# Optimization experiments

Hardware: AMD Instinct MI355X
Metric: run time of the kernel (lower is better)

The kernel has to match this reference:

```python
import jax, jax.numpy as jnp
import numpy as np

NUM_USR = 8192
H = 256  # NUM_SOURCE == H (feature dim of y_a); NUM_TARGET = 256


def setup_inputs() -> dict:
    key = jax.random.key(0)
    k1, k2, k3, k4 = jax.random.split(key, 4)
    return {
        "y_a": jax.random.normal(k1, (NUM_USR, H), dtype=jnp.float32),
        "y_b": jax.random.normal(k2, (NUM_USR, H), dtype=jnp.float32),
        "W": jax.random.normal(k3, (H, H), dtype=jnp.float32) * (1.0 / np.sqrt(H)),
        "b": jax.random.normal(k4, (H,), dtype=jnp.float32) * 0.01,
    }


def reference(y_a, y_b, W, b):
    # Linear: proj[j] = W @ y_b[j] + b   (torch nn.Linear convention)
    proj = jnp.einsum("jt,st->js", y_b, W) + b          # [num_usr, H]
    # torch loop computes score[i, j] = y_a[i] . proj[j], replicated H times
    # then averaged: out[i, k] = (1/H) * sum_j sigmoid(score[i, j])
    scores = jnp.einsum("ih,jh->ij", y_a, proj)          # [num_usr, num_usr]
    s = jnp.sum(jax.nn.sigmoid(scores), axis=1) / y_a.shape[1]  # [num_usr]
    return jnp.broadcast_to(s[:, None], y_a.shape)       # [num_usr, H]
```

## Files before the change

### kernel.cpp

```cpp
#include <hip/hip_runtime.h>

#define NUSR 8192
#define HDIM 256

typedef __attribute__((ext_vector_type(8))) __bf16 bf16x8;
typedef __attribute__((ext_vector_type(4))) float f32x4;

union frag_u { bf16x8 v; unsigned short u[8]; unsigned int d[4]; };

__device__ __forceinline__ unsigned int f2bf(float f) {
  unsigned u = __builtin_bit_cast(unsigned, f);
  u += 0x7FFFu + ((u >> 16) & 1u);
  return u >> 16;
}
__device__ __forceinline__ unsigned int f2bf2(float lo, float hi) {
  return f2bf(lo) | (f2bf(hi) << 16);
}
__device__ __forceinline__ float sigmoidf_fast(float x) {
  float e = __builtin_amdgcn_exp2f(x * -1.44269504088896340736f);
  return __builtin_amdgcn_rcpf(1.0f + e);
}


__global__ __launch_bounds__(256) void k1_fused(
    const float* __restrict__ ya, const float* __restrict__ yb,
    const float* __restrict__ W, const float* __restrict__ bvec,
    unsigned short* __restrict__ yabf, unsigned short* __restrict__ PX,
    float* __restrict__ svec, unsigned int* __restrict__ done)
{
  const int b   = blockIdx.x;
  const int tid = threadIdx.x;

  if (b < 128) {
    const int lane = tid & 63;
    const int w    = tid >> 6;
    const int q    = lane >> 4;
    const int i    = lane & 15;

    frag_u B[4][8];
#pragma unroll
    for (int g = 0; g < 4; ++g) {
      const float* ybrow = yb + (size_t)(b * 64 + g * 16 + i) * HDIM;
#pragma unroll
      for (int kb = 0; kb < 8; ++kb) {
        float4 v0 = *(const float4*)&ybrow[kb * 32 + q * 8];
        float4 v1 = *(const float4*)&ybrow[kb * 32 + q * 8 + 4];
        B[g][kb].d[0] = f2bf2(v0.x, v0.y); B[g][kb].d[1] = f2bf2(v0.z, v0.w);
        B[g][kb].d[2] = f2bf2(v1.x, v1.y); B[g][kb].d[3] = f2bf2(v1.z, v1.w);
      }
    }

#pragma unroll
    for (int t = 0; t < 4; ++t) {
      const int st = w * 4 + t;
      f32x4 acc[4] = {{0.f,0.f,0.f,0.f},{0.f,0.f,0.f,0.f},
                      {0.f,0.f,0.f,0.f},{0.f,0.f,0.f,0.f}};
#pragma unroll
      for (int kb = 0; kb < 8; ++kb) {
        const float* wr = W + (size_t)(st * 16 + i) * HDIM + kb * 32 + q * 8;
        float4 w0 = *(const float4*)wr;
        float4 w1 = *(const float4*)(wr + 4);
        frag_u Af;
        Af.d[0] = f2bf2(w0.x, w0.y); Af.d[1] = f2bf2(w0.z, w0.w);
        Af.d[2] = f2bf2(w1.x, w1.y); Af.d[3] = f2bf2(w1.z, w1.w);
#pragma unroll
        for (int g = 0; g < 4; ++g)
          acc[g] = __builtin_amdgcn_mfma_f32_16x16x32_bf16(Af.v, B[g][kb].v, acc[g], 0, 0, 0);
      }
      float4 bias = *(const float4*)&bvec[st * 16 + q * 4];
#pragma unroll
      for (int g = 0; g < 4; ++g) {
        const int jg = b * 4 + g;
        unsigned v0 = f2bf2(acc[g][0] + bias.x, acc[g][1] + bias.y);
        unsigned v1 = f2bf2(acc[g][2] + bias.z, acc[g][3] + bias.w);
        size_t off = (size_t)jg * 4096 + (size_t)(st >> 1) * 512
                   + (size_t)(((st & 1) << 1) | (q >> 1)) * 128 + i * 8 + ((q & 1) * 4);
        *(uint2*)(PX + off) = make_uint2(v0, v1);
      }
    }
  } else {
    const int id = (b - 128) * 256 + tid;
    const float4* src = (const float4*)ya;
    uint4* dst = (uint4*)yabf;
#pragma unroll
    for (int u = 0; u < 3; ++u) {
      int d = id + u * 98304;
      if (d < 262144) {
        float4 a = src[d * 2];
        float4 c = src[d * 2 + 1];
        uint4 o = { f2bf2(a.x, a.y), f2bf2(a.z, a.w),
                    f2bf2(c.x, c.y), f2bf2(c.z, c.w) };
        dst[d] = o;
      }
    }
    if (b == 511) {
      float4 z = {0.f, 0.f, 0.f, 0.f};
      float4* sv = (float4*)svec;
#pragma unroll
      for (int u = 0; u < 8; ++u) sv[u * 256 + tid] = z;
      if (tid < 32) done[tid] = 0u;
    }
  }
}

__global__ __launch_bounds__(256, 2) void k2_score(
    const unsigned short* __restrict__ yabf, const unsigned short* __restrict__ PX,
    float* __restrict__ svec, unsigned int* __restrict__ done,
    float* __restrict__ out, const int fuse_tail)
{
  __shared__ __align__(16) unsigned short bs[2][8192];
  __shared__ unsigned int lastv;
  const int tid  = threadIdx.x;
  const int lane = tid & 63;
  const int w    = tid >> 6;
  const int quad = lane >> 4;
  const int l15  = lane & 15;
  const int rbase = blockIdx.x * 256 + w * 64;
  const int cg16  = blockIdx.y * 32;

  frag_u A[4][8];
#pragma unroll
  for (int g = 0; g < 4; ++g) {
    const unsigned short* src = yabf + (size_t)(rbase + g * 16 + l15) * HDIM;
#pragma unroll
    for (int kb = 0; kb < 8; ++kb)
      A[g][kb].v = *(const bf16x8*)&src[kb * 32 + quad * 8];
  }

  const unsigned short* psrc = PX + (size_t)cg16 * 4096;

  float rs[4][4] = {{0.f,0.f,0.f,0.f},{0.f,0.f,0.f,0.f},
                    {0.f,0.f,0.f,0.f},{0.f,0.f,0.f,0.f}};

#pragma unroll
  for (int p = 0; p < 4; ++p) {
    int c = p * 256 + tid;
    __builtin_amdgcn_global_load_lds(
        (const __attribute__((address_space(1))) unsigned int*)(const void*)(psrc + c * 8),
        (__attribute__((address_space(3))) unsigned int*)(void*)(&bs[0][0] + c * 8),
        16, 0, 0);
  }
  __syncthreads();

  for (int t = 0; t < 16; ++t) {
    if (t < 15) {
      const unsigned short* src = psrc + (size_t)(t + 1) * 8192;
      unsigned short* dst = &bs[(t + 1) & 1][0];
#pragma unroll
      for (int p = 0; p < 4; ++p) {
        int c = p * 256 + tid;
        __builtin_amdgcn_global_load_lds(
            (const __attribute__((address_space(1))) unsigned int*)(const void*)(src + c * 8),
            (__attribute__((address_space(3))) unsigned int*)(void*)(dst + c * 8),
            16, 0, 0);
      }
    }
    const unsigned short* buf = &bs[t & 1][0];
#pragma unroll
    for (int tt = 0; tt < 2; ++tt) {
      f32x4 acc[4] = {{0.f,0.f,0.f,0.f},{0.f,0.f,0.f,0.f},
                      {0.f,0.f,0.f,0.f},{0.f,0.f,0.f,0.f}};
#pragma unroll
      for (int kb = 0; kb < 8; ++kb) {
        bf16x8 bfrag = *(const bf16x8*)&buf[(tt * 512 + kb * 64 + lane) * 8];
#pragma unroll
        for (int g = 0; g < 4; ++g)
          acc[g] = __builtin_amdgcn_mfma_f32_16x16x32_bf16(A[g][kb].v, bfrag, acc[g], 0, 0, 0);
      }
#pragma unroll
      for (int g = 0; g < 4; ++g)
#pragma unroll
        for (int r = 0; r < 4; ++r)
          rs[g][r] += sigmoidf_fast(acc[g][r]);
    }
    __syncthreads();
  }

#pragma unroll
  for (int off = 1; off < 16; off <<= 1)
#pragma unroll
    for (int g = 0; g < 4; ++g)
#pragma unroll
      for (int r = 0; r < 4; ++r)
        rs[g][r] += __shfl_xor(rs[g][r], off, 64);

  if (l15 == 0) {
#pragma unroll
    for (int g = 0; g < 4; ++g)
#pragma unroll
      for (int r = 0; r < 4; ++r)
        atomicAdd(&svec[rbase + g * 16 + quad * 4 + r], rs[g][r]);
  }

  if (!fuse_tail) return;

  __syncthreads();
  if (tid == 0)
    lastv = __hip_atomic_fetch_add(&done[blockIdx.x], 1u,
                                   __ATOMIC_ACQ_REL, __HIP_MEMORY_SCOPE_AGENT);
  __syncthreads();
  if (lastv == 15u) {
    const int rb = blockIdx.x * 256;
    const float inv = 1.0f / 256.0f;
#pragma unroll 4
    for (int u = 0; u < 64; ++u) {
      int row = u * 4 + w;
      float s = __hip_atomic_load(&svec[rb + row],
                                  __ATOMIC_RELAXED, __HIP_MEMORY_SCOPE_AGENT);
      float v = s * inv;
      float4 o = {v, v, v, v};
      ((float4*)out)[(size_t)(rb + row) * 64 + lane] = o;
    }
  }
}

__global__ __launch_bounds__(256) void k3_bcast(
    const float* __restrict__ svec, float* __restrict__ out)
{
  int idx = blockIdx.x * 256 + threadIdx.x;
  int row = idx >> 6;
  float v = svec[row] * (1.0f / 256.0f);
  float4 o = {v, v, v, v};
  ((float4*)out)[idx] = o;
}

extern "C" void kernel_launch(void* const* d_in, const int* in_sizes, int n_in,
                              void* d_out, int out_size, void* d_ws, size_t ws_size,
                              hipStream_t stream) {
  (void)in_sizes; (void)n_in; (void)out_size;
  const float* ya = (const float*)d_in[0];
  const float* yb = (const float*)d_in[1];
  const float* W  = (const float*)d_in[2];
  const float* bv = (const float*)d_in[3];
  float* out = (float*)d_out;

  char* ws = (char*)d_ws;
  unsigned short *PX, *yabf;
  float* svec;
  unsigned int* done;
  int fuse;
  const size_t need = (8ull << 20) + (64ull << 10);
  if (ws_size >= need) {
    PX   = (unsigned short*)ws;
    yabf = (unsigned short*)(ws + (4 << 20));
    svec = (float*)(ws + (8 << 20));
    done = (unsigned int*)(ws + (8 << 20) + (32 << 10));
    fuse = 1;
  } else {
    PX   = (unsigned short*)d_out;
    yabf = (unsigned short*)((char*)d_out + (4 << 20));
    svec = (float*)ws;
    done = (unsigned int*)(ws + (32 << 10));
    fuse = 0;
  }

  k1_fused<<<512, 256, 0, stream>>>(ya, yb, W, bv, yabf, PX, svec, done);
  k2_score<<<dim3(32, 16), 256, 0, stream>>>(yabf, PX, svec, done, out, fuse);
  if (!fuse) k3_bcast<<<2048, 256, 0, stream>>>(svec, out);
}
```

Baseline: 138.7 us.

## Load score-kernel B fragments directly to registers, remap blocks per XCD, drop fused tail

```diff
diff --git a/kernel.cpp b/kernel.cpp
--- a/kernel.cpp
+++ b/kernel.cpp
@@ -26,21 +26,21 @@
     const float* __restrict__ ya, const float* __restrict__ yb,
     const float* __restrict__ W, const float* __restrict__ bvec,
     unsigned short* __restrict__ yabf, unsigned short* __restrict__ PX,
-    float* __restrict__ svec, unsigned int* __restrict__ done)
+    float* __restrict__ svec)
 {
   const int b   = blockIdx.x;
   const int tid = threadIdx.x;
 
-  if (b < 128) {
+  if (b < 256) {
     const int lane = tid & 63;
     const int w    = tid >> 6;
     const int q    = lane >> 4;
     const int i    = lane & 15;
 
-    frag_u B[4][8];
-#pragma unroll
-    for (int g = 0; g < 4; ++g) {
-      const float* ybrow = yb + (size_t)(b * 64 + g * 16 + i) * HDIM;
+    frag_u B[2][8];
+#pragma unroll
+    for (int g = 0; g < 2; ++g) {
+      const float* ybrow = yb + (size_t)(b * 32 + g * 16 + i) * HDIM;
 #pragma unroll
       for (int kb = 0; kb < 8; ++kb) {
         float4 v0 = *(const float4*)&ybrow[kb * 32 + q * 8];
@@ -53,8 +53,7 @@
 #pragma unroll
     for (int t = 0; t < 4; ++t) {
       const int st = w * 4 + t;
-      f32x4 acc[4] = {{0.f,0.f,0.f,0.f},{0.f,0.f,0.f,0.f},
-                      {0.f,0.f,0.f,0.f},{0.f,0.f,0.f,0.f}};
+      f32x4 acc[2] = {{0.f,0.f,0.f,0.f},{0.f,0.f,0.f,0.f}};
 #pragma unroll
       for (int kb = 0; kb < 8; ++kb) {
         const float* wr = W + (size_t)(st * 16 + i) * HDIM + kb * 32 + q * 8;
@@ -64,13 +63,13 @@
         Af.d[0] = f2bf2(w0.x, w0.y); Af.d[1] = f2bf2(w0.z, w0.w);
         Af.d[2] = f2bf2(w1.x, w1.y); Af.d[3] = f2bf2(w1.z, w1.w);
 #pragma unroll
-        for (int g = 0; g < 4; ++g)
+        for (int g = 0; g < 2; ++g)
           acc[g] = __builtin_amdgcn_mfma_f32_16x16x32_bf16(Af.v, B[g][kb].v, acc[g], 0, 0, 0);
       }
       float4 bias = *(const float4*)&bvec[st * 16 + q * 4];
 #pragma unroll
-      for (int g = 0; g < 4; ++g) {
-        const int jg = b * 4 + g;
+      for (int g = 0; g < 2; ++g) {
+        const int jg = b * 2 + g;
         unsigned v0 = f2bf2(acc[g][0] + bias.x, acc[g][1] + bias.y);
         unsigned v1 = f2bf2(acc[g][2] + bias.z, acc[g][3] + bias.w);
         size_t off = (size_t)jg * 4096 + (size_t)(st >> 1) * 512
@@ -79,44 +78,45 @@
       }
     }
   } else {
-    const int id = (b - 128) * 256 + tid;
+    const int id = (b - 256) * 256 + tid;
     const float4* src = (const float4*)ya;
     uint4* dst = (uint4*)yabf;
 #pragma unroll
-    for (int u = 0; u < 3; ++u) {
-      int d = id + u * 98304;
-      if (d < 262144) {
-        float4 a = src[d * 2];
-        float4 c = src[d * 2 + 1];
-        uint4 o = { f2bf2(a.x, a.y), f2bf2(a.z, a.w),
-                    f2bf2(c.x, c.y), f2bf2(c.z, c.w) };
-        dst[d] = o;
-      }
+    for (int u = 0; u < 4; ++u) {
+      int d = id + u * 65536;
+      float4 a = src[d * 2];
+      float4 c = src[d * 2 + 1];
+      uint4 o = { f2bf2(a.x, a.y), f2bf2(a.z, a.w),
+                  f2bf2(c.x, c.y), f2bf2(c.z, c.w) };
+      dst[d] = o;
     }
     if (b == 511) {
       float4 z = {0.f, 0.f, 0.f, 0.f};
       float4* sv = (float4*)svec;
 #pragma unroll
       for (int u = 0; u < 8; ++u) sv[u * 256 + tid] = z;
-      if (tid < 32) done[tid] = 0u;
     }
   }
 }
 
 __global__ __launch_bounds__(256, 2) void k2_score(
     const unsigned short* __restrict__ yabf, const unsigned short* __restrict__ PX,
-    float* __restrict__ svec, unsigned int* __restrict__ done,
-    float* __restrict__ out, const int fuse_tail)
+    float* __restrict__ svec)
 {
-  __shared__ __align__(16) unsigned short bs[2][8192];
-  __shared__ unsigned int lastv;
   const int tid  = threadIdx.x;
   const int lane = tid & 63;
   const int w    = tid >> 6;
   const int quad = lane >> 4;
   const int l15  = lane & 15;
-  const int rbase = blockIdx.x * 256 + w * 64;
-  const int cg16  = blockIdx.y * 32;
+
+  const int bid = blockIdx.x;
+  const int xcd = bid & 7;
+  const int k   = bid >> 3;
+  const int by  = xcd * 2 + (k >> 5);
+  const int bx  = k & 31;
+
+  const int rbase = bx * 256 + w * 64;
+  const int cg16  = by * 32;
 
   frag_u A[4][8];
 #pragma unroll
@@ -132,49 +132,45 @@
   float rs[4][4] = {{0.f,0.f,0.f,0.f},{0.f,0.f,0.f,0.f},
                     {0.f,0.f,0.f,0.f},{0.f,0.f,0.f,0.f}};
 
-#pragma unroll
-  for (int p = 0; p < 4; ++p) {
-    int c = p * 256 + tid;
-    __builtin_amdgcn_global_load_lds(
-        (const __attribute__((address_space(1))) unsigned int*)(const void*)(psrc + c * 8),
-        (__attribute__((address_space(3))) unsigned int*)(void*)(&bs[0][0] + c * 8),
-        16, 0, 0);
-  }
-  __syncthreads();
+  frag_u Ba[8], Bb[8];
+
+#define LOADSEG(DST, SEG)                                                   \
+  do {                                                                      \
+    const unsigned short* _s = psrc + (size_t)(SEG) * 4096;                 \
+    _Pragma("unroll")                                                       \
+    for (int kb = 0; kb < 8; ++kb)                                          \
+      DST[kb].v = *(const bf16x8*)&_s[kb * 512 + lane * 8];                 \
+  } while (0)
+
+#define COMPUTESEG(BUF)                                                     \
+  do {                                                                      \
+    f32x4 acc[4] = {{0.f,0.f,0.f,0.f},{0.f,0.f,0.f,0.f},                    \
+                    {0.f,0.f,0.f,0.f},{0.f,0.f,0.f,0.f}};                   \
+    _Pragma("unroll")                                                       \
+    for (int kb = 0; kb < 8; ++kb) {                                        \
+      _Pragma("unroll")                                                     \
+      for (int g = 0; g < 4; ++g)                                           \
+        acc[g] = __builtin_amdgcn_mfma_f32_16x16x32_bf16(                   \
+            A[g][kb].v, BUF[kb].v, acc[g], 0, 0, 0);                        \
+    }                                                                       \
+    _Pragma("unroll")                                                       \
+    for (int g = 0; g < 4; ++g)                                             \
+      _Pragma("unroll")                                                     \
+      for (int r = 0; r < 4; ++r)                                           \
+        rs[g][r] += sigmoidf_fast(acc[g][r]);                               \
+  } while (0)
+
+  LOADSEG(Ba, 0);
 
   for (int t = 0; t < 16; ++t) {
-    if (t < 15) {
-      const unsigned short* src = psrc + (size_t)(t + 1) * 8192;
-      unsigned short* dst = &bs[(t + 1) & 1][0];
-#pragma unroll
-      for (int p = 0; p < 4; ++p) {
-        int c = p * 256 + tid;
-        __builtin_amdgcn_global_load_lds(
-            (const __attribute__((address_space(1))) unsigned int*)(const void*)(src + c * 8),
-            (__attribute__((address_space(3))) unsigned int*)(void*)(dst + c * 8),
-            16, 0, 0);
-      }
-    }
-    const unsigned short* buf = &bs[t & 1][0];
-#pragma unroll
-    for (int tt = 0; tt < 2; ++tt) {
-      f32x4 acc[4] = {{0.f,0.f,0.f,0.f},{0.f,0.f,0.f,0.f},
-                      {0.f,0.f,0.f,0.f},{0.f,0.f,0.f,0.f}};
-#pragma unroll
-      for (int kb = 0; kb < 8; ++kb) {
-        bf16x8 bfrag = *(const bf16x8*)&buf[(tt * 512 + kb * 64 + lane) * 8];
-#pragma unroll
-        for (int g = 0; g < 4; ++g)
-          acc[g] = __builtin_amdgcn_mfma_f32_16x16x32_bf16(A[g][kb].v, bfrag, acc[g], 0, 0, 0);
-      }
-#pragma unroll
-      for (int g = 0; g < 4; ++g)
-#pragma unroll
-        for (int r = 0; r < 4; ++r)
-          rs[g][r] += sigmoidf_fast(acc[g][r]);
-    }
-    __syncthreads();
-  }
+    LOADSEG(Bb, 2 * t + 1);
+    COMPUTESEG(Ba);
+    if (t < 15)
+      LOADSEG(Ba, 2 * t + 2);
+    COMPUTESEG(Bb);
+  }
+#undef LOADSEG
+#undef COMPUTESEG
 
 #pragma unroll
   for (int off = 1; off < 16; off <<= 1)
@@ -190,27 +186,6 @@
 #pragma unroll
       for (int r = 0; r < 4; ++r)
         atomicAdd(&svec[rbase + g * 16 + quad * 4 + r], rs[g][r]);
-  }
-
-  if (!fuse_tail) return;
-
-  __syncthreads();
-  if (tid == 0)
-    lastv = __hip_atomic_fetch_add(&done[blockIdx.x], 1u,
-                                   __ATOMIC_ACQ_REL, __HIP_MEMORY_SCOPE_AGENT);
-  __syncthreads();
-  if (lastv == 15u) {
-    const int rb = blockIdx.x * 256;
-    const float inv = 1.0f / 256.0f;
-#pragma unroll 4
-    for (int u = 0; u < 64; ++u) {
-      int row = u * 4 + w;
-      float s = __hip_atomic_load(&svec[rb + row],
-                                  __ATOMIC_RELAXED, __HIP_MEMORY_SCOPE_AGENT);
-      float v = s * inv;
-      float4 o = {v, v, v, v};
-      ((float4*)out)[(size_t)(rb + row) * 64 + lane] = o;
-    }
   }
 }
 
@@ -237,24 +212,18 @@
   char* ws = (char*)d_ws;
   unsigned short *PX, *yabf;
   float* svec;
-  unsigned int* done;
-  int fuse;
-  const size_t need = (8ull << 20) + (64ull << 10);
+  const size_t need = (8ull << 20) + (32ull << 10);
   if (ws_size >= need) {
     PX   = (unsigned short*)ws;
     yabf = (unsigned short*)(ws + (4 << 20));
     svec = (float*)(ws + (8 << 20));
-    done = (unsigned int*)(ws + (8 << 20) + (32 << 10));
-    fuse = 1;
   } else {
     PX   = (unsigned short*)d_out;
     yabf = (unsigned short*)((char*)d_out + (4 << 20));
     svec = (float*)ws;
-    done = (unsigned int*)(ws + (32 << 10));
-    fuse = 0;
-  }
-
-  k1_fused<<<512, 256, 0, stream>>>(ya, yb, W, bv, yabf, PX, svec, done);
-  k2_score<<<dim3(32, 16), 256, 0, stream>>>(yabf, PX, svec, done, out, fuse);
-  if (!fuse) k3_bcast<<<2048, 256, 0, stream>>>(svec, out);
-}
+  }
+
+  k1_fused<<<512, 256, 0, stream>>>(ya, yb, W, bv, yabf, PX, svec);
+  k2_score<<<512, 256, 0, stream>>>(yabf, PX, svec);
+  k3_bcast<<<2048, 256, 0, stream>>>(svec, out);
+}
```

Result: faster. 120.3 us (-13.2%).
